# Performance work log

Hardware: AMD Instinct MI355X
Metric: run time of the kernel (lower is better)

## Reference

```python
import jax, jax.numpy as jnp
import numpy as np


def setup_inputs() -> dict:
    key = jax.random.key(0)
    ks = jax.random.split(key, 8)
    B, T, N = 8, 8192, 256
    x = jax.random.normal(ks[0], (B, T, N), dtype=jnp.float32)
    # stable-ish LRU params: nu_log/theta_log as in the torch init
    u1 = jax.random.uniform(ks[1], (N,), dtype=jnp.float32)
    r_min, r_max = 0.4, 0.9
    nu_log = jnp.log(-0.5 * jnp.log(u1 * (r_max + r_min) * (r_max - r_min) + r_min ** 2))
    u2 = jax.random.uniform(ks[2], (N,), dtype=jnp.float32)
    theta_log = jnp.log(2.0 * np.pi * u2)
    L_mod = jnp.exp(-jnp.exp(nu_log))
    gamma_log = jnp.log(jnp.sqrt(1.0 - jnp.square(L_mod)))
    s2 = 1.0 / np.sqrt(2 * N)
    s1 = 1.0 / np.sqrt(N)
    B_re = jax.random.normal(ks[3], (N, N), dtype=jnp.float32) * s2
    B_im = jax.random.normal(ks[4], (N, N), dtype=jnp.float32) * s2
    C_re = jax.random.normal(ks[5], (N, N), dtype=jnp.float32) * s1
    C_im = jax.random.normal(ks[6], (N, N), dtype=jnp.float32) * s1
    return {"x": x, "nu_log": nu_log, "theta_log": theta_log, "gamma_log": gamma_log,
            "B_re": B_re, "B_im": B_im, "C_re": C_re, "C_im": C_im}


def _binop(e_i, e_j):
    # associative combine for diagonal linear recurrence h_j = a_j * h_i + b_j
    a_i, b_i = e_i
    a_j, b_j = e_j
    return a_j * a_i, a_j * b_i + b_j


def reference(x, nu_log, theta_log, gamma_log, B_re, B_im, C_re, C_im):
    # Lambda (diagonal complex state transition)
    L_mod = jnp.exp(-jnp.exp(nu_log))                     # [N]
    theta = jnp.exp(theta_log)                            # [N]
    L_diag = (L_mod * jnp.cos(theta) + 1j * (L_mod * jnp.sin(theta)))  # complex64 [N]
    # normalized input projection
    B_norm = (B_re + 1j * B_im) * jnp.exp(gamma_log)[:, None]          # [N, N]
    Bu = jnp.einsum('btn,mn->btm', x.astype(B_norm.dtype), B_norm)     # [B, T, N] complex
    L_elems = jnp.broadcast_to(L_diag, Bu.shape)                        # [B, T, N]
    # parallel associative scan over time axis (zero initial state)
    _, states = jax.lax.associative_scan(_binop, (L_elems, Bu), axis=1)
    C = C_re + 1j * C_im
    return jnp.einsum('btn,mn->btm', states, C).real
```

## Files before the change

### kernel.cpp

```cpp
#include <hip/hip_runtime.h>

#define NB 8
#define TT 8192
#define NN 256
#define BT (NB*TT)
#define CH 64
#define NCHUNK (BT/CH)
#define GPB (TT/CH)

typedef float f4 __attribute__((ext_vector_type(4)));
typedef unsigned u4 __attribute__((ext_vector_type(4)));
typedef short b8 __attribute__((ext_vector_type(8)));

static __device__ __forceinline__ ushort f2bf(float f) {
  union { float f; unsigned u; } v; v.f = f;
  return (ushort)((v.u + 0x7fffu + ((v.u >> 16) & 1u)) >> 16);
}
static __device__ __forceinline__ float bf2f(ushort h) {
  union { unsigned u; float f; } v; v.u = ((unsigned)h) << 16; return v.f;
}

__global__ void k_setup(const float* __restrict__ nu_log, const float* __restrict__ theta_log,
                        const float* __restrict__ gamma_log,
                        const float* __restrict__ B_re, const float* __restrict__ B_im,
                        const float* __restrict__ C_re, const float* __restrict__ C_im,
                        float2* __restrict__ Lc, float2* __restrict__ LCH,
                        float2* __restrict__ Lpow,
                        ushort* __restrict__ BnRe, ushort* __restrict__ BnIm,
                        ushort* __restrict__ CRe, ushort* __restrict__ CIm) {
  int bid = blockIdx.x, tid = threadIdx.x;
  if (bid < NN) {
    int m = bid, n = tid;
    float g = expf(gamma_log[m]);
    int idx = m * NN + n;
    BnRe[idx] = f2bf(B_re[idx] * g);
    BnIm[idx] = f2bf(B_im[idx] * g);
    CRe[idx]  = f2bf(C_re[idx]);
    CIm[idx]  = f2bf(-C_im[idx]);
  } else {
    int m = tid;
    float Lmod = expf(-expf(nu_log[m]));
    float th = expf(theta_log[m]);
    float lre = Lmod * cosf(th), lim = Lmod * sinf(th);
    Lc[m] = make_float2(lre, lim);
    float pr = 1.f, pi = 0.f;
    for (int k = 0; k < CH; ++k) {
      Lpow[(size_t)(CH - 1 - k) * NN + m] = make_float2(pr, pi);
      float npr = pr * lre - pi * lim;
      pi = pr * lim + pi * lre;
      pr = npr;
    }
    LCH[m] = make_float2(pr, pi);
  }
}

static __device__ __forceinline__ void stage_x_f32(const float* __restrict__ xt,
                                                   char* lds, int tid) {
#pragma unroll
  for (int i = 0; i < 16; ++i) {
    int fi = i * 1024 + tid * 4;
    f4 w = *(const f4*)(xt + fi);
    int r = fi >> 8, c = fi & 255;
    int dst = r * 1024 + ((c * 4) ^ ((r & 7) << 4));
    *(f4*)(lds + dst) = w;
  }
}

static __device__ __forceinline__ void gemm1_ldsx(const char* lds,
                                                  const ushort* __restrict__ BnRe,
                                                  const ushort* __restrict__ BnIm,
                                                  int tid, f4 accRe[4][4], f4 accIm[4][4]) {
  int lane = tid & 63, wid = tid >> 6;
  int lr = lane & 15, lg = lane >> 4;
  int mq = wid * 64;
  for (int ks = 0; ks < 8; ++ks) {
    int k0 = ks * 32 + lg * 8;
    b8 a[4];
    for (int mf = 0; mf < 4; ++mf) {
      int r = mf * 16 + lr;
      int sw = (r & 7) << 4;
      const char* base = lds + r * 1024;
      f4 x0 = *(const f4*)(base + ((k0 * 4) ^ sw));
      f4 x1 = *(const f4*)(base + ((k0 * 4 + 16) ^ sw));
      b8 t;
      t[0] = (short)f2bf(x0[0]); t[1] = (short)f2bf(x0[1]);
      t[2] = (short)f2bf(x0[2]); t[3] = (short)f2bf(x0[3]);
      t[4] = (short)f2bf(x1[0]); t[5] = (short)f2bf(x1[1]);
      t[6] = (short)f2bf(x1[2]); t[7] = (short)f2bf(x1[3]);
      a[mf] = t;
    }
    for (int nf = 0; nf < 4; ++nf) {
      int mrow = mq + nf * 16 + lr;
      b8 br = *(const b8*)(BnRe + (size_t)mrow * NN + k0);
      b8 bi = *(const b8*)(BnIm + (size_t)mrow * NN + k0);
      for (int mf = 0; mf < 4; ++mf) {
        accRe[mf][nf] = __builtin_amdgcn_mfma_f32_16x16x32_bf16(a[mf], br, accRe[mf][nf], 0, 0, 0);
        accIm[mf][nf] = __builtin_amdgcn_mfma_f32_16x16x32_bf16(a[mf], bi, accIm[mf][nf], 0, 0, 0);
      }
    }
  }
}

__global__ __launch_bounds__(256) void k_carry(const float* __restrict__ x,
                                               const ushort* __restrict__ BnRe,
                                               const ushort* __restrict__ BnIm,
                                               const float2* __restrict__ Lpow,
                                               float2* __restrict__ carry) {
  __shared__ char lds[65536];
  int cid = blockIdx.x, tid = threadIdx.x;
  int lane = tid & 63, wid = tid >> 6;
  int lr = lane & 15, lg = lane >> 4;
  int mq = wid * 64;

  stage_x_f32(x + (size_t)cid * CH * NN, lds, tid);
  __syncthreads();

  f4 accRe[4][4], accIm[4][4];
  for (int i = 0; i < 4; ++i)
    for (int j = 0; j < 4; ++j) { accRe[i][j] = (f4)0.f; accIm[i][j] = (f4)0.f; }
  gemm1_ldsx(lds, BnRe, BnIm, tid, accRe, accIm);

  for (int nf = 0; nf < 4; ++nf) {
    int col = mq + nf * 16 + lr;
    float sr = 0.f, si = 0.f;
    for (int mf = 0; mf < 4; ++mf)
      for (int q = 0; q < 4; ++q) {
        int t = mf * 16 + lg * 4 + q;
        float2 w = Lpow[(size_t)t * NN + col];
        float br = accRe[mf][nf][q], bi = accIm[mf][nf][q];
        sr += w.x * br - w.y * bi;
        si += w.x * bi + w.y * br;
      }
    sr += __shfl_xor(sr, 16, 64);  si += __shfl_xor(si, 16, 64);
    sr += __shfl_xor(sr, 32, 64);  si += __shfl_xor(si, 32, 64);
    if (lg == 0) carry[(size_t)cid * NN + col] = make_float2(sr, si);
  }
}

__global__ void k_seed(float2* __restrict__ carrySeed, const float2* __restrict__ LCH) {
  int b = blockIdx.x, m = threadIdx.x;
  float2 LC = LCH[m];
  float hr = 0.f, hi = 0.f;
  size_t base = (size_t)b * GPB * NN + m;
  float2 c = carrySeed[base];
  for (int g = 0; g < GPB; ++g) {
    size_t idx = base + (size_t)g * NN;
    float2 cn = (g + 1 < GPB) ? carrySeed[idx + NN] : make_float2(0.f, 0.f);
    carrySeed[idx] = make_float2(hr, hi);
    float nr = LC.x * hr - LC.y * hi + c.x;
    hi = LC.x * hi + LC.y * hr + c.y;
    hr = nr;
    c = cn;
  }
}

__global__ __launch_bounds__(256) void k_out(const float* __restrict__ x,
                                             const ushort* __restrict__ BnRe,
                                             const ushort* __restrict__ BnIm,
                                             const float2* __restrict__ Lc,
                                             const float2* __restrict__ seed,
                                             const ushort* __restrict__ CRe,
                                             const ushort* __restrict__ CIm,
                                             float* __restrict__ out) {
  __shared__ char lds[65536];
  int cid = blockIdx.x, tid = threadIdx.x;
  size_t rowbase = (size_t)cid * CH;
  int lane = tid & 63, wid = tid >> 6;
  int lr = lane & 15, lg = lane >> 4;
  int mq = wid * 64;

  stage_x_f32(x + rowbase * NN, lds, tid);
  __syncthreads();

  f4 accRe[4][4], accIm[4][4];
  for (int i = 0; i < 4; ++i)
    for (int j = 0; j < 4; ++j) { accRe[i][j] = (f4)0.f; accIm[i][j] = (f4)0.f; }
  gemm1_ldsx(lds, BnRe, BnIm, tid, accRe, accIm);
  __syncthreads();

  for (int mf = 0; mf < 4; ++mf)
    for (int nf = 0; nf < 4; ++nf)
      for (int r = 0; r < 4; ++r) {
        int row = mf * 16 + lg * 4 + r;
        int col = mq + nf * 16 + lr;
        unsigned p = (unsigned)f2bf(accRe[mf][nf][r]) | ((unsigned)f2bf(accIm[mf][nf][r]) << 16);
        int off = row * 1024 + ((col * 4) ^ ((row & 7) << 4));
        *(unsigned*)(lds + off) = p;
      }
  __syncthreads();

  {
    int c = tid;
    float2 L = Lc[c];
    float2 s = seed[(size_t)cid * NN + c];
    float hr = s.x, hi = s.y;
    for (int k = 0; k < CH; ++k) {
      int off = k * 1024 + ((c * 4) ^ ((k & 7) << 4));
      unsigned u = *(const unsigned*)(lds + off);
      float ur = bf2f((ushort)(u & 0xffffu)), ui = bf2f((ushort)(u >> 16));
      float nr = L.x * hr - L.y * hi + ur;
      hi = L.x * hi + L.y * hr + ui;
      hr = nr;
      *(unsigned*)(lds + off) = (unsigned)f2bf(hr) | ((unsigned)f2bf(hi) << 16);
    }
  }
  __syncthreads();

  f4 acc[4][4];
  for (int i = 0; i < 4; ++i)
    for (int j = 0; j < 4; ++j) acc[i][j] = (f4)0.f;

  for (int ks = 0; ks < 8; ++ks) {
    int k0 = ks * 32 + lg * 8;
    b8 ar[4], ai[4];
    for (int mf = 0; mf < 4; ++mf) {
      int row = mf * 16 + lr;
      int m4 = (row & 7) << 4;
      const char* base = lds + row * 1024;
      u4 p0 = *(const u4*)(base + ((k0 * 4) ^ m4));
      u4 p1 = *(const u4*)(base + ((k0 * 4 + 16) ^ m4));
      b8 tr, ti;
      tr[0] = (short)(p0[0] & 0xffffu); ti[0] = (short)(p0[0] >> 16);
      tr[1] = (short)(p0[1] & 0xffffu); ti[1] = (short)(p0[1] >> 16);
      tr[2] = (short)(p0[2] & 0xffffu); ti[2] = (short)(p0[2] >> 16);
      tr[3] = (short)(p0[3] & 0xffffu); ti[3] = (short)(p0[3] >> 16);
      tr[4] = (short)(p1[0] & 0xffffu); ti[4] = (short)(p1[0] >> 16);
      tr[5] = (short)(p1[1] & 0xffffu); ti[5] = (short)(p1[1] >> 16);
      tr[6] = (short)(p1[2] & 0xffffu); ti[6] = (short)(p1[2] >> 16);
      tr[7] = (short)(p1[3] & 0xffffu); ti[7] = (short)(p1[3] >> 16);
      ar[mf] = tr; ai[mf] = ti;
    }
    for (int nf = 0; nf < 4; ++nf) {
      int m = mq + nf * 16 + lr;
      b8 cr = *(const b8*)(CRe + (size_t)m * NN + k0);
      b8 ci = *(const b8*)(CIm + (size_t)m * NN + k0);
      for (int mf = 0; mf < 4; ++mf) {
        acc[mf][nf] = __builtin_amdgcn_mfma_f32_16x16x32_bf16(ar[mf], cr, acc[mf][nf], 0, 0, 0);
        acc[mf][nf] = __builtin_amdgcn_mfma_f32_16x16x32_bf16(ai[mf], ci, acc[mf][nf], 0, 0, 0);
      }
    }
  }
  for (int mf = 0; mf < 4; ++mf)
    for (int nf = 0; nf < 4; ++nf)
      for (int r = 0; r < 4; ++r) {
        size_t t = rowbase + mf * 16 + lg * 4 + r;
        out[t * NN + mq + nf * 16 + lr] = acc[mf][nf][r];
      }
}

extern "C" void kernel_launch(void* const* d_in, const int* in_sizes, int n_in,
                              void* d_out, int out_size, void* d_ws, size_t ws_size,
                              hipStream_t stream) {
  const float* x         = (const float*)d_in[0];
  const float* nu_log    = (const float*)d_in[1];
  const float* theta_log = (const float*)d_in[2];
  const float* gamma_log = (const float*)d_in[3];
  const float* B_re      = (const float*)d_in[4];
  const float* B_im      = (const float*)d_in[5];
  const float* C_re      = (const float*)d_in[6];
  const float* C_im      = (const float*)d_in[7];
  float* out = (float*)d_out;

  char* ws = (char*)d_ws;
  float2*  carrySeed = (float2*)(ws + 0);
  float2*  Lc   = (float2*)(ws + 2097152);
  float2*  LCH  = (float2*)(ws + 2099200);
  ushort*  BnRe = (ushort*)(ws + 2101248);
  ushort*  BnIm = (ushort*)(ws + 2232320);
  ushort*  CRe  = (ushort*)(ws + 2363392);
  ushort*  CIm  = (ushort*)(ws + 2494464);
  float2*  Lpow = (float2*)(ws + 2625536);

  hipLaunchKernelGGL(k_setup, dim3(NN + 1), dim3(NN), 0, stream,
                     nu_log, theta_log, gamma_log, B_re, B_im, C_re, C_im,
                     Lc, LCH, Lpow, BnRe, BnIm, CRe, CIm);
  hipLaunchKernelGGL(k_carry, dim3(NCHUNK), dim3(256), 0, stream,
                     x, BnRe, BnIm, Lpow, carrySeed);
  hipLaunchKernelGGL(k_seed, dim3(NB), dim3(NN), 0, stream, carrySeed, LCH);
  hipLaunchKernelGGL(k_out, dim3(NCHUNK), dim3(256), 0, stream,
                     x, BnRe, BnIm, Lc, carrySeed, CRe, CIm, out);
}
```

Before: 179.1 us.

## Process each 64-row chunk as two 32-row sub-tiles to halve LDS and registers

Both the carry and output kernels now loop over two 32-row sub-tiles per chunk instead of handling all 64 rows at once. LDS drops from 64KB to 32KB and the accumulator arrays shrink by half. The scan state and carry partial sums are carried across sub-tiles. This aims to raise occupancy (more blocks per CU) at the cost of extra barriers, and B/C weight fragments are now reloaded from global memory twice per chunk.

```diff
diff --git a/kernel.cpp b/kernel.cpp
--- a/kernel.cpp
+++ b/kernel.cpp
@@ -3,8 +3,9 @@
 #define NB 8
 #define TT 8192
 #define NN 256
+#define CH 64
+#define SUB 32
 #define BT (NB*TT)
-#define CH 64
 #define NCHUNK (BT/CH)
 #define GPB (TT/CH)
 
@@ -57,7 +58,7 @@
 static __device__ __forceinline__ void stage_x_f32(const float* __restrict__ xt,
                                                    char* lds, int tid) {
 #pragma unroll
-  for (int i = 0; i < 16; ++i) {
+  for (int i = 0; i < 8; ++i) {
     int fi = i * 1024 + tid * 4;
     f4 w = *(const f4*)(xt + fi);
     int r = fi >> 8, c = fi & 255;
@@ -69,14 +70,14 @@
 static __device__ __forceinline__ void gemm1_ldsx(const char* lds,
                                                   const ushort* __restrict__ BnRe,
                                                   const ushort* __restrict__ BnIm,
-                                                  int tid, f4 accRe[4][4], f4 accIm[4][4]) {
+                                                  int tid, f4 accRe[2][4], f4 accIm[2][4]) {
   int lane = tid & 63, wid = tid >> 6;
   int lr = lane & 15, lg = lane >> 4;
   int mq = wid * 64;
   for (int ks = 0; ks < 8; ++ks) {
     int k0 = ks * 32 + lg * 8;
-    b8 a[4];
-    for (int mf = 0; mf < 4; ++mf) {
+    b8 a[2];
+    for (int mf = 0; mf < 2; ++mf) {
       int r = mf * 16 + lr;
       int sw = (r & 7) << 4;
       const char* base = lds + r * 1024;
@@ -93,7 +94,7 @@
       int mrow = mq + nf * 16 + lr;
       b8 br = *(const b8*)(BnRe + (size_t)mrow * NN + k0);
       b8 bi = *(const b8*)(BnIm + (size_t)mrow * NN + k0);
-      for (int mf = 0; mf < 4; ++mf) {
+      for (int mf = 0; mf < 2; ++mf) {
         accRe[mf][nf] = __builtin_amdgcn_mfma_f32_16x16x32_bf16(a[mf], br, accRe[mf][nf], 0, 0, 0);
         accIm[mf][nf] = __builtin_amdgcn_mfma_f32_16x16x32_bf16(a[mf], bi, accIm[mf][nf], 0, 0, 0);
       }
@@ -106,34 +107,44 @@
                                                const ushort* __restrict__ BnIm,
                                                const float2* __restrict__ Lpow,
                                                float2* __restrict__ carry) {
-  __shared__ char lds[65536];
+  __shared__ char lds[SUB * 1024];
   int cid = blockIdx.x, tid = threadIdx.x;
   int lane = tid & 63, wid = tid >> 6;
   int lr = lane & 15, lg = lane >> 4;
   int mq = wid * 64;
 
-  stage_x_f32(x + (size_t)cid * CH * NN, lds, tid);
-  __syncthreads();
-
-  f4 accRe[4][4], accIm[4][4];
-  for (int i = 0; i < 4; ++i)
-    for (int j = 0; j < 4; ++j) { accRe[i][j] = (f4)0.f; accIm[i][j] = (f4)0.f; }
-  gemm1_ldsx(lds, BnRe, BnIm, tid, accRe, accIm);
+  float sr[4] = {0.f, 0.f, 0.f, 0.f}, si[4] = {0.f, 0.f, 0.f, 0.f};
+
+#pragma unroll 1
+  for (int sub = 0; sub < 2; ++sub) {
+    __syncthreads();
+    stage_x_f32(x + ((size_t)cid * CH + sub * SUB) * NN, lds, tid);
+    __syncthreads();
+
+    f4 accRe[2][4], accIm[2][4];
+    for (int i = 0; i < 2; ++i)
+      for (int j = 0; j < 4; ++j) { accRe[i][j] = (f4)0.f; accIm[i][j] = (f4)0.f; }
+    gemm1_ldsx(lds, BnRe, BnIm, tid, accRe, accIm);
+
+    for (int nf = 0; nf < 4; ++nf) {
+      int col = mq + nf * 16 + lr;
+      for (int mf = 0; mf < 2; ++mf)
+        for (int q = 0; q < 4; ++q) {
+          int t = sub * SUB + mf * 16 + lg * 4 + q;
+          float2 w = Lpow[(size_t)t * NN + col];
+          float br = accRe[mf][nf][q], bi = accIm[mf][nf][q];
+          sr[nf] += w.x * br - w.y * bi;
+          si[nf] += w.x * bi + w.y * br;
+        }
+    }
+  }
 
   for (int nf = 0; nf < 4; ++nf) {
     int col = mq + nf * 16 + lr;
-    float sr = 0.f, si = 0.f;
-    for (int mf = 0; mf < 4; ++mf)
-      for (int q = 0; q < 4; ++q) {
-        int t = mf * 16 + lg * 4 + q;
-        float2 w = Lpow[(size_t)t * NN + col];
-        float br = accRe[mf][nf][q], bi = accIm[mf][nf][q];
-        sr += w.x * br - w.y * bi;
-        si += w.x * bi + w.y * br;
-      }
-    sr += __shfl_xor(sr, 16, 64);  si += __shfl_xor(si, 16, 64);
-    sr += __shfl_xor(sr, 32, 64);  si += __shfl_xor(si, 32, 64);
-    if (lg == 0) carry[(size_t)cid * NN + col] = make_float2(sr, si);
+    float r = sr[nf], m = si[nf];
+    r += __shfl_xor(r, 16, 64);  m += __shfl_xor(m, 16, 64);
+    r += __shfl_xor(r, 32, 64);  m += __shfl_xor(m, 32, 64);
+    if (lg == 0) carry[(size_t)cid * NN + col] = make_float2(r, m);
   }
 }
 
@@ -162,90 +173,95 @@
                                              const ushort* __restrict__ CRe,
                                              const ushort* __restrict__ CIm,
                                              float* __restrict__ out) {
-  __shared__ char lds[65536];
+  __shared__ char lds[SUB * 1024];
   int cid = blockIdx.x, tid = threadIdx.x;
-  size_t rowbase = (size_t)cid * CH;
   int lane = tid & 63, wid = tid >> 6;
   int lr = lane & 15, lg = lane >> 4;
   int mq = wid * 64;
 
-  stage_x_f32(x + rowbase * NN, lds, tid);
-  __syncthreads();
-
-  f4 accRe[4][4], accIm[4][4];
-  for (int i = 0; i < 4; ++i)
-    for (int j = 0; j < 4; ++j) { accRe[i][j] = (f4)0.f; accIm[i][j] = (f4)0.f; }
-  gemm1_ldsx(lds, BnRe, BnIm, tid, accRe, accIm);
-  __syncthreads();
-
-  for (int mf = 0; mf < 4; ++mf)
-    for (int nf = 0; nf < 4; ++nf)
-      for (int r = 0; r < 4; ++r) {
-        int row = mf * 16 + lg * 4 + r;
-        int col = mq + nf * 16 + lr;
-        unsigned p = (unsigned)f2bf(accRe[mf][nf][r]) | ((unsigned)f2bf(accIm[mf][nf][r]) << 16);
-        int off = row * 1024 + ((col * 4) ^ ((row & 7) << 4));
-        *(unsigned*)(lds + off) = p;
-      }
-  __syncthreads();
-
-  {
-    int c = tid;
-    float2 L = Lc[c];
-    float2 s = seed[(size_t)cid * NN + c];
-    float hr = s.x, hi = s.y;
-    for (int k = 0; k < CH; ++k) {
-      int off = k * 1024 + ((c * 4) ^ ((k & 7) << 4));
-      unsigned u = *(const unsigned*)(lds + off);
-      float ur = bf2f((ushort)(u & 0xffffu)), ui = bf2f((ushort)(u >> 16));
-      float nr = L.x * hr - L.y * hi + ur;
-      hi = L.x * hi + L.y * hr + ui;
-      hr = nr;
-      *(unsigned*)(lds + off) = (unsigned)f2bf(hr) | ((unsigned)f2bf(hi) << 16);
-    }
-  }
-  __syncthreads();
-
-  f4 acc[4][4];
-  for (int i = 0; i < 4; ++i)
-    for (int j = 0; j < 4; ++j) acc[i][j] = (f4)0.f;
-
-  for (int ks = 0; ks < 8; ++ks) {
-    int k0 = ks * 32 + lg * 8;
-    b8 ar[4], ai[4];
-    for (int mf = 0; mf < 4; ++mf) {
-      int row = mf * 16 + lr;
-      int m4 = (row & 7) << 4;
-      const char* base = lds + row * 1024;
-      u4 p0 = *(const u4*)(base + ((k0 * 4) ^ m4));
-      u4 p1 = *(const u4*)(base + ((k0 * 4 + 16) ^ m4));
-      b8 tr, ti;
-      tr[0] = (short)(p0[0] & 0xffffu); ti[0] = (short)(p0[0] >> 16);
-      tr[1] = (short)(p0[1] & 0xffffu); ti[1] = (short)(p0[1] >> 16);
-      tr[2] = (short)(p0[2] & 0xffffu); ti[2] = (short)(p0[2] >> 16);
-      tr[3] = (short)(p0[3] & 0xffffu); ti[3] = (short)(p0[3] >> 16);
-      tr[4] = (short)(p1[0] & 0xffffu); ti[4] = (short)(p1[0] >> 16);
-      tr[5] = (short)(p1[1] & 0xffffu); ti[5] = (short)(p1[1] >> 16);
-      tr[6] = (short)(p1[2] & 0xffffu); ti[6] = (short)(p1[2] >> 16);
-      tr[7] = (short)(p1[3] & 0xffffu); ti[7] = (short)(p1[3] >> 16);
-      ar[mf] = tr; ai[mf] = ti;
-    }
-    for (int nf = 0; nf < 4; ++nf) {
-      int m = mq + nf * 16 + lr;
-      b8 cr = *(const b8*)(CRe + (size_t)m * NN + k0);
-      b8 ci = *(const b8*)(CIm + (size_t)m * NN + k0);
-      for (int mf = 0; mf < 4; ++mf) {
-        acc[mf][nf] = __builtin_amdgcn_mfma_f32_16x16x32_bf16(ar[mf], cr, acc[mf][nf], 0, 0, 0);
-        acc[mf][nf] = __builtin_amdgcn_mfma_f32_16x16x32_bf16(ai[mf], ci, acc[mf][nf], 0, 0, 0);
-      }
-    }
-  }
-  for (int mf = 0; mf < 4; ++mf)
-    for (int nf = 0; nf < 4; ++nf)
-      for (int r = 0; r < 4; ++r) {
-        size_t t = rowbase + mf * 16 + lg * 4 + r;
-        out[t * NN + mq + nf * 16 + lr] = acc[mf][nf][r];
-      }
+  float2 L = Lc[tid];
+  float2 s = seed[(size_t)cid * NN + tid];
+  float hr = s.x, hi = s.y;
+
+#pragma unroll 1
+  for (int sub = 0; sub < 2; ++sub) {
+    size_t rowbase = (size_t)cid * CH + sub * SUB;
+    __syncthreads();
+    stage_x_f32(x + rowbase * NN, lds, tid);
+    __syncthreads();
+
+    f4 accRe[2][4], accIm[2][4];
+    for (int i = 0; i < 2; ++i)
+      for (int j = 0; j < 4; ++j) { accRe[i][j] = (f4)0.f; accIm[i][j] = (f4)0.f; }
+    gemm1_ldsx(lds, BnRe, BnIm, tid, accRe, accIm);
+    __syncthreads();
+
+    for (int mf = 0; mf < 2; ++mf)
+      for (int nf = 0; nf < 4; ++nf)
+        for (int r = 0; r < 4; ++r) {
+          int row = mf * 16 + lg * 4 + r;
+          int col = mq + nf * 16 + lr;
+          unsigned p = (unsigned)f2bf(accRe[mf][nf][r]) | ((unsigned)f2bf(accIm[mf][nf][r]) << 16);
+          int off = row * 1024 + ((col * 4) ^ ((row & 7) << 4));
+          *(unsigned*)(lds + off) = p;
+        }
+    __syncthreads();
+
+    {
+      int c = tid;
+      for (int k = 0; k < SUB; ++k) {
+        int off = k * 1024 + ((c * 4) ^ ((k & 7) << 4));
+        unsigned u = *(const unsigned*)(lds + off);
+        float ur = bf2f((ushort)(u & 0xffffu)), ui = bf2f((ushort)(u >> 16));
+        float nr = L.x * hr - L.y * hi + ur;
+        hi = L.x * hi + L.y * hr + ui;
+        hr = nr;
+        *(unsigned*)(lds + off) = (unsigned)f2bf(hr) | ((unsigned)f2bf(hi) << 16);
+      }
+    }
+    __syncthreads();
+
+    f4 acc[2][4];
+    for (int i = 0; i < 2; ++i)
+      for (int j = 0; j < 4; ++j) acc[i][j] = (f4)0.f;
+
+    for (int ks = 0; ks < 8; ++ks) {
+      int k0 = ks * 32 + lg * 8;
+      b8 ar[2], ai[2];
+      for (int mf = 0; mf < 2; ++mf) {
+        int row = mf * 16 + lr;
+        int m4 = (row & 7) << 4;
+        const char* base = lds + row * 1024;
+        u4 p0 = *(const u4*)(base + ((k0 * 4) ^ m4));
+        u4 p1 = *(const u4*)(base + ((k0 * 4 + 16) ^ m4));
+        b8 tr, ti;
+        tr[0] = (short)(p0[0] & 0xffffu); ti[0] = (short)(p0[0] >> 16);
+        tr[1] = (short)(p0[1] & 0xffffu); ti[1] = (short)(p0[1] >> 16);
+        tr[2] = (short)(p0[2] & 0xffffu); ti[2] = (short)(p0[2] >> 16);
+        tr[3] = (short)(p0[3] & 0xffffu); ti[3] = (short)(p0[3] >> 16);
+        tr[4] = (short)(p1[0] & 0xffffu); ti[4] = (short)(p1[0] >> 16);
+        tr[5] = (short)(p1[1] & 0xffffu); ti[5] = (short)(p1[1] >> 16);
+        tr[6] = (short)(p1[2] & 0xffffu); ti[6] = (short)(p1[2] >> 16);
+        tr[7] = (short)(p1[3] & 0xffffu); ti[7] = (short)(p1[3] >> 16);
+        ar[mf] = tr; ai[mf] = ti;
+      }
+      for (int nf = 0; nf < 4; ++nf) {
+        int m = mq + nf * 16 + lr;
+        b8 cr = *(const b8*)(CRe + (size_t)m * NN + k0);
+        b8 ci = *(const b8*)(CIm + (size_t)m * NN + k0);
+        for (int mf = 0; mf < 2; ++mf) {
+          acc[mf][nf] = __builtin_amdgcn_mfma_f32_16x16x32_bf16(ar[mf], cr, acc[mf][nf], 0, 0, 0);
+          acc[mf][nf] = __builtin_amdgcn_mfma_f32_16x16x32_bf16(ai[mf], ci, acc[mf][nf], 0, 0, 0);
+        }
+      }
+    }
+    for (int mf = 0; mf < 2; ++mf)
+      for (int nf = 0; nf < 4; ++nf)
+        for (int r = 0; r < 4; ++r) {
+          size_t t = rowbase + mf * 16 + lg * 4 + r;
+          out[t * NN + mq + nf * 16 + lr] = acc[mf][nf][r];
+        }
+  }
 }
 
 extern "C" void kernel_launch(void* const* d_in, const int* in_sizes, int n_in,
```

Result: slower. 395.3 us (+120.7%).

## Fuse carry, seed and output kernels into single-pass chained scan with decoupled lookback

Applied to the files above, without the earlier changes.

Replaces the three-kernel chunked scan (carry, sequential seed, output) with one kernel. Each block takes a chunk index from an atomic ticket, computes its local carry, spins on the previous chunk's published prefix state, then publishes its own. The point is to drop the second GEMM1 pass over x and the serial seed kernel, at the cost of a serial chain of inter-block waits across 128 chunks per batch. The spin-wait relies on ticket ordering to avoid deadlock, and setup now also fills the payload buffer with a sentinel value.

```diff
diff --git a/kernel.cpp b/kernel.cpp
--- a/kernel.cpp
+++ b/kernel.cpp
@@ -3,14 +3,16 @@
 #define NB 8
 #define TT 8192
 #define NN 256
+#define CH 64
 #define BT (NB*TT)
-#define CH 64
 #define NCHUNK (BT/CH)
 #define GPB (TT/CH)
+#define SENTINEL 0xFFFFFFFFFFFFFFFFull
 
 typedef float f4 __attribute__((ext_vector_type(4)));
 typedef unsigned u4 __attribute__((ext_vector_type(4)));
 typedef short b8 __attribute__((ext_vector_type(8)));
+typedef unsigned long long u64;
 
 static __device__ __forceinline__ ushort f2bf(float f) {
   union { float f; unsigned u; } v; v.f = f;
@@ -24,11 +26,15 @@
                         const float* __restrict__ gamma_log,
                         const float* __restrict__ B_re, const float* __restrict__ B_im,
                         const float* __restrict__ C_re, const float* __restrict__ C_im,
-                        float2* __restrict__ Lc, float2* __restrict__ LCH,
-                        float2* __restrict__ Lpow,
+                        float2* __restrict__ Pow, unsigned* __restrict__ ticket,
+                        u64* __restrict__ payload,
                         ushort* __restrict__ BnRe, ushort* __restrict__ BnIm,
                         ushort* __restrict__ CRe, ushort* __restrict__ CIm) {
   int bid = blockIdx.x, tid = threadIdx.x;
+  for (int k = 0; k < 4; ++k) {
+    int idx = (bid * 256 + tid) * 4 + k;
+    if (idx < NCHUNK * NN) payload[idx] = SENTINEL;
+  }
   if (bid < NN) {
     int m = bid, n = tid;
     float g = expf(gamma_log[m]);
@@ -38,19 +44,18 @@
     CRe[idx]  = f2bf(C_re[idx]);
     CIm[idx]  = f2bf(-C_im[idx]);
   } else {
+    if (tid == 0) *ticket = 0;
     int m = tid;
     float Lmod = expf(-expf(nu_log[m]));
     float th = expf(theta_log[m]);
     float lre = Lmod * cosf(th), lim = Lmod * sinf(th);
-    Lc[m] = make_float2(lre, lim);
     float pr = 1.f, pi = 0.f;
-    for (int k = 0; k < CH; ++k) {
-      Lpow[(size_t)(CH - 1 - k) * NN + m] = make_float2(pr, pi);
+    for (int j = 1; j <= CH; ++j) {
       float npr = pr * lre - pi * lim;
       pi = pr * lim + pi * lre;
       pr = npr;
-    }
-    LCH[m] = make_float2(pr, pi);
+      Pow[(size_t)(j - 1) * NN + m] = make_float2(pr, pi);
+    }
   }
 }
 
@@ -101,18 +106,30 @@
   }
 }
 
-__global__ __launch_bounds__(256) void k_carry(const float* __restrict__ x,
+__global__ __launch_bounds__(256) void k_fused(const float* __restrict__ x,
                                                const ushort* __restrict__ BnRe,
                                                const ushort* __restrict__ BnIm,
-                                               const float2* __restrict__ Lpow,
-                                               float2* __restrict__ carry) {
-  __shared__ char lds[65536];
-  int cid = blockIdx.x, tid = threadIdx.x;
+                                               const ushort* __restrict__ CRe,
+                                               const ushort* __restrict__ CIm,
+                                               const float2* __restrict__ Pow,
+                                               unsigned* ticket, u64* payload,
+                                               float* __restrict__ out) {
+  __shared__ char lds[CH * 1024];
+  __shared__ int s_cid;
+  int tid = threadIdx.x;
   int lane = tid & 63, wid = tid >> 6;
   int lr = lane & 15, lg = lane >> 4;
   int mq = wid * 64;
 
-  stage_x_f32(x + (size_t)cid * CH * NN, lds, tid);
+  if (tid == 0)
+    s_cid = (int)(__hip_atomic_fetch_add(ticket, 1u, __ATOMIC_RELAXED,
+                                         __HIP_MEMORY_SCOPE_AGENT) & (NCHUNK - 1));
+  __syncthreads();
+  int cid = s_cid;
+  int g = cid & (GPB - 1);
+  size_t rowbase = (size_t)cid * CH;
+
+  stage_x_f32(x + rowbase * NN, lds, tid);
   __syncthreads();
 
   f4 accRe[4][4], accIm[4][4];
@@ -120,62 +137,52 @@
     for (int j = 0; j < 4; ++j) { accRe[i][j] = (f4)0.f; accIm[i][j] = (f4)0.f; }
   gemm1_ldsx(lds, BnRe, BnIm, tid, accRe, accIm);
 
+  float lcr[4], lci[4];
   for (int nf = 0; nf < 4; ++nf) {
     int col = mq + nf * 16 + lr;
     float sr = 0.f, si = 0.f;
     for (int mf = 0; mf < 4; ++mf)
       for (int q = 0; q < 4; ++q) {
         int t = mf * 16 + lg * 4 + q;
-        float2 w = Lpow[(size_t)t * NN + col];
+        float2 w = (t == CH - 1) ? make_float2(1.f, 0.f)
+                                 : Pow[(size_t)(CH - 2 - t) * NN + col];
         float br = accRe[mf][nf][q], bi = accIm[mf][nf][q];
         sr += w.x * br - w.y * bi;
         si += w.x * bi + w.y * br;
       }
     sr += __shfl_xor(sr, 16, 64);  si += __shfl_xor(si, 16, 64);
     sr += __shfl_xor(sr, 32, 64);  si += __shfl_xor(si, 32, 64);
-    if (lg == 0) carry[(size_t)cid * NN + col] = make_float2(sr, si);
-  }
-}
-
-__global__ void k_seed(float2* __restrict__ carrySeed, const float2* __restrict__ LCH) {
-  int b = blockIdx.x, m = threadIdx.x;
-  float2 LC = LCH[m];
-  float hr = 0.f, hi = 0.f;
-  size_t base = (size_t)b * GPB * NN + m;
-  float2 c = carrySeed[base];
-  for (int g = 0; g < GPB; ++g) {
-    size_t idx = base + (size_t)g * NN;
-    float2 cn = (g + 1 < GPB) ? carrySeed[idx + NN] : make_float2(0.f, 0.f);
-    carrySeed[idx] = make_float2(hr, hi);
-    float nr = LC.x * hr - LC.y * hi + c.x;
-    hi = LC.x * hi + LC.y * hr + c.y;
-    hr = nr;
-    c = cn;
-  }
-}
-
-__global__ __launch_bounds__(256) void k_out(const float* __restrict__ x,
-                                             const ushort* __restrict__ BnRe,
-                                             const ushort* __restrict__ BnIm,
-                                             const float2* __restrict__ Lc,
-                                             const float2* __restrict__ seed,
-                                             const ushort* __restrict__ CRe,
-                                             const ushort* __restrict__ CIm,
-                                             float* __restrict__ out) {
-  __shared__ char lds[65536];
-  int cid = blockIdx.x, tid = threadIdx.x;
-  size_t rowbase = (size_t)cid * CH;
-  int lane = tid & 63, wid = tid >> 6;
-  int lr = lane & 15, lg = lane >> 4;
-  int mq = wid * 64;
-
-  stage_x_f32(x + rowbase * NN, lds, tid);
-  __syncthreads();
-
-  f4 accRe[4][4], accIm[4][4];
-  for (int i = 0; i < 4; ++i)
-    for (int j = 0; j < 4; ++j) { accRe[i][j] = (f4)0.f; accIm[i][j] = (f4)0.f; }
-  gemm1_ldsx(lds, BnRe, BnIm, tid, accRe, accIm);
+    lcr[nf] = sr; lci[nf] = si;
+  }
+
+  float2 seed = make_float2(0.f, 0.f);
+  if (g > 0) {
+    u64 v; int it = 0;
+    do {
+      v = __hip_atomic_load(&payload[(size_t)(cid - 1) * NN + tid],
+                            __ATOMIC_RELAXED, __HIP_MEMORY_SCOPE_AGENT);
+      if (v != SENTINEL) break;
+      __builtin_amdgcn_s_sleep(2);
+    } while (++it < (1 << 24));
+    union { u64 u; float2 f; } cv; cv.u = v;
+    seed = cv.f;
+  }
+
+  if (g < GPB - 1) {
+    for (int nf = 0; nf < 4; ++nf) {
+      int col = mq + nf * 16 + lr;
+      float sx = __shfl(seed.x, col & 63, 64);
+      float sy = __shfl(seed.y, col & 63, 64);
+      if (lg == 0) {
+        float2 LC = Pow[(size_t)(CH - 1) * NN + col];
+        union { float2 f; u64 u; } ov;
+        ov.f = make_float2(LC.x * sx - LC.y * sy + lcr[nf],
+                           LC.x * sy + LC.y * sx + lci[nf]);
+        __hip_atomic_store(&payload[(size_t)cid * NN + col], ov.u,
+                           __ATOMIC_RELAXED, __HIP_MEMORY_SCOPE_AGENT);
+      }
+    }
+  }
   __syncthreads();
 
   for (int mf = 0; mf < 4; ++mf)
@@ -191,9 +198,8 @@
 
   {
     int c = tid;
-    float2 L = Lc[c];
-    float2 s = seed[(size_t)cid * NN + c];
-    float hr = s.x, hi = s.y;
+    float2 L = Pow[c];
+    float hr = seed.x, hi = seed.y;
     for (int k = 0; k < CH; ++k) {
       int off = k * 1024 + ((c * 4) ^ ((k & 7) << 4));
       unsigned u = *(const unsigned*)(lds + off);
@@ -262,21 +268,17 @@
   float* out = (float*)d_out;
 
   char* ws = (char*)d_ws;
-  float2*  carrySeed = (float2*)(ws + 0);
-  float2*  Lc   = (float2*)(ws + 2097152);
-  float2*  LCH  = (float2*)(ws + 2099200);
-  ushort*  BnRe = (ushort*)(ws + 2101248);
-  ushort*  BnIm = (ushort*)(ws + 2232320);
-  ushort*  CRe  = (ushort*)(ws + 2363392);
-  ushort*  CIm  = (ushort*)(ws + 2494464);
-  float2*  Lpow = (float2*)(ws + 2625536);
+  u64*      payload = (u64*)(ws + 0);
+  unsigned* ticket  = (unsigned*)(ws + 2097152);
+  float2*   Pow     = (float2*)(ws + 2097408);
+  ushort*   BnRe    = (ushort*)(ws + 2228480);
+  ushort*   BnIm    = (ushort*)(ws + 2359552);
+  ushort*   CRe     = (ushort*)(ws + 2490624);
+  ushort*   CIm     = (ushort*)(ws + 2621696);
 
   hipLaunchKernelGGL(k_setup, dim3(NN + 1), dim3(NN), 0, stream,
                      nu_log, theta_log, gamma_log, B_re, B_im, C_re, C_im,
-                     Lc, LCH, Lpow, BnRe, BnIm, CRe, CIm);
-  hipLaunchKernelGGL(k_carry, dim3(NCHUNK), dim3(256), 0, stream,
-                     x, BnRe, BnIm, Lpow, carrySeed);
-  hipLaunchKernelGGL(k_seed, dim3(NB), dim3(NN), 0, stream, carrySeed, LCH);
-  hipLaunchKernelGGL(k_out, dim3(NCHUNK), dim3(256), 0, stream,
-                     x, BnRe, BnIm, Lc, carrySeed, CRe, CIm, out);
-}
+                     Pow, ticket, payload, BnRe, BnIm, CRe, CIm);
+  hipLaunchKernelGGL(k_fused, dim3(NCHUNK), dim3(256), 0, stream,
+                     x, BnRe, BnIm, CRe, CIm, Pow, ticket, payload, out);
+}
```

Result: slower. 597.8 us (+233.8%).

## Replace serial per-chunk LDS scan with in-register parallel scan over MFMA accumulators

Applied to the files above, without the earlier changes.

The 64-step sequential recurrence in k_out, which read and wrote bf16 values through LDS one time step at a time, is replaced by a scan done directly on the GEMM accumulator fragments. Each lane scans its four rows locally, then lanes combine across the four 16-lane groups with shuffles using precomputed powers of Lambda, and the chunk seed is folded in. This removes a serial LDS loop and one barrier, and it keeps the intermediate state in fp32 rather than rounding to bf16 at every step. In exchange it adds shuffle and complex-multiply work and extra Lpow loads per thread.

```diff
diff --git a/kernel.cpp b/kernel.cpp
--- a/kernel.cpp
+++ b/kernel.cpp
@@ -3,8 +3,8 @@
 #define NB 8
 #define TT 8192
 #define NN 256
+#define CH 64
 #define BT (NB*TT)
-#define CH 64
 #define NCHUNK (BT/CH)
 #define GPB (TT/CH)
 
@@ -161,6 +161,7 @@
                                              const float2* __restrict__ seed,
                                              const ushort* __restrict__ CRe,
                                              const ushort* __restrict__ CIm,
+                                             const float2* __restrict__ Lpow,
                                              float* __restrict__ out) {
   __shared__ char lds[65536];
   int cid = blockIdx.x, tid = threadIdx.x;
@@ -176,6 +177,58 @@
   for (int i = 0; i < 4; ++i)
     for (int j = 0; j < 4; ++j) { accRe[i][j] = (f4)0.f; accIm[i][j] = (f4)0.f; }
   gemm1_ldsx(lds, BnRe, BnIm, tid, accRe, accIm);
+
+  for (int nf = 0; nf < 4; ++nf) {
+    int c = mq + nf * 16 + lr;
+    float2 L1  = Lc[c];
+    float2 L4  = Lpow[(size_t)(CH - 1 - 4)  * NN + c];
+    float2 L8  = Lpow[(size_t)(CH - 1 - 8)  * NN + c];
+    float2 L16 = Lpow[(size_t)(CH - 1 - 16) * NN + c];
+    float2 w4  = (lg == 0) ? make_float2(1.f, 0.f)
+                           : Lpow[(size_t)(CH - 1 - 4 * lg) * NN + c];
+    float2 sd  = seed[(size_t)cid * NN + c];
+
+    float Cr[4], Ci[4];
+    for (int mf = 0; mf < 4; ++mf) {
+      for (int q = 1; q < 4; ++q) {
+        float sr_ = L1.x * accRe[mf][nf][q-1] - L1.y * accIm[mf][nf][q-1] + accRe[mf][nf][q];
+        float si_ = L1.x * accIm[mf][nf][q-1] + L1.y * accRe[mf][nf][q-1] + accIm[mf][nf][q];
+        accRe[mf][nf][q] = sr_; accIm[mf][nf][q] = si_;
+      }
+      Cr[mf] = accRe[mf][nf][3]; Ci[mf] = accIm[mf][nf][3];
+    }
+
+    float Er[4], Ei[4], Qr[4], Qi[4];
+    for (int mf = 0; mf < 4; ++mf) {
+      float tx = __shfl_up(Cr[mf], 16, 64), ty = __shfl_up(Ci[mf], 16, 64);
+      float m1 = (lg >= 1) ? 1.f : 0.f;
+      float ax = Cr[mf] + m1 * (L4.x * tx - L4.y * ty);
+      float ay = Ci[mf] + m1 * (L4.x * ty + L4.y * tx);
+      float ux = __shfl_up(ax, 32, 64), uy = __shfl_up(ay, 32, 64);
+      float m2 = (lg >= 2) ? 1.f : 0.f;
+      float Ix = ax + m2 * (L8.x * ux - L8.y * uy);
+      float Iy = ay + m2 * (L8.x * uy + L8.y * ux);
+      float ex = __shfl_up(Ix, 16, 64), ey = __shfl_up(Iy, 16, 64);
+      Er[mf] = m1 * ex; Ei[mf] = m1 * ey;
+      Qr[mf] = __shfl(Ix, lr + 48, 64); Qi[mf] = __shfl(Iy, lr + 48, 64);
+    }
+
+    float Hx = sd.x, Hy = sd.y;
+    for (int mf = 0; mf < 4; ++mf) {
+      float Zx = Er[mf] + w4.x * Hx - w4.y * Hy;
+      float Zy = Ei[mf] + w4.x * Hy + w4.y * Hx;
+      float Wx = L1.x, Wy = L1.y;
+      for (int q = 0; q < 4; ++q) {
+        float hr_ = accRe[mf][nf][q] + Wx * Zx - Wy * Zy;
+        float hi_ = accIm[mf][nf][q] + Wx * Zy + Wy * Zx;
+        accRe[mf][nf][q] = hr_; accIm[mf][nf][q] = hi_;
+        if (q < 3) { float nWx = Wx * L1.x - Wy * L1.y; Wy = Wx * L1.y + Wy * L1.x; Wx = nWx; }
+      }
+      float nHx = Qr[mf] + L16.x * Hx - L16.y * Hy;
+      Hy = Qi[mf] + L16.x * Hy + L16.y * Hx;
+      Hx = nHx;
+    }
+  }
   __syncthreads();
 
   for (int mf = 0; mf < 4; ++mf)
@@ -187,23 +240,6 @@
         int off = row * 1024 + ((col * 4) ^ ((row & 7) << 4));
         *(unsigned*)(lds + off) = p;
       }
-  __syncthreads();
-
-  {
-    int c = tid;
-    float2 L = Lc[c];
-    float2 s = seed[(size_t)cid * NN + c];
-    float hr = s.x, hi = s.y;
-    for (int k = 0; k < CH; ++k) {
-      int off = k * 1024 + ((c * 4) ^ ((k & 7) << 4));
-      unsigned u = *(const unsigned*)(lds + off);
-      float ur = bf2f((ushort)(u & 0xffffu)), ui = bf2f((ushort)(u >> 16));
-      float nr = L.x * hr - L.y * hi + ur;
-      hi = L.x * hi + L.y * hr + ui;
-      hr = nr;
-      *(unsigned*)(lds + off) = (unsigned)f2bf(hr) | ((unsigned)f2bf(hi) << 16);
-    }
-  }
   __syncthreads();
 
   f4 acc[4][4];
@@ -278,5 +314,5 @@
                      x, BnRe, BnIm, Lpow, carrySeed);
   hipLaunchKernelGGL(k_seed, dim3(NB), dim3(NN), 0, stream, carrySeed, LCH);
   hipLaunchKernelGGL(k_out, dim3(NCHUNK), dim3(256), 0, stream,
-                     x, BnRe, BnIm, Lc, carrySeed, CRe, CIm, out);
-}
+                     x, BnRe, BnIm, Lc, carrySeed, CRe, CIm, Lpow, out);
+}
```

New measurement: 177.1 us. Within noise of the previous version (-1.1%).
